# Performance work log

Hardware: AMD Instinct MI355X
Metric: run time of the kernel (lower is better)

The kernel has to match this reference:

```python
import jax, jax.numpy as jnp
import numpy as np

G = 64      # num graphs
N = 1024    # nodes per graph (equal-sized graphs)
D_IN, D_H, D_OUT = 128, 256, 10


def setup_inputs() -> dict:
    key = jax.random.key(0)
    k1, k2, k3, k4, k5 = jax.random.split(key, 5)
    x = jax.random.normal(k1, (G * N, D_IN), dtype=jnp.float32)
    batch = jnp.repeat(jnp.arange(G, dtype=jnp.int64), N)  # sorted graph ids
    lim1 = 1.0 / np.sqrt(D_IN)
    lim2 = 1.0 / np.sqrt(D_H)
    W1 = jax.random.uniform(k2, (D_IN, D_H), minval=-lim1, maxval=lim1, dtype=jnp.float32)
    b1 = jax.random.uniform(k3, (D_H,), minval=-lim1, maxval=lim1, dtype=jnp.float32)
    W2 = jax.random.uniform(k4, (D_H, D_OUT), minval=-lim2, maxval=lim2, dtype=jnp.float32)
    b2 = jax.random.uniform(k5, (D_OUT,), minval=-lim2, maxval=lim2, dtype=jnp.float32)
    return {"x": x, "batch": batch, "W1": W1, "b1": b1, "W2": W2, "b2": b2}


def reference(x, batch, W1, b1, W2, b2):
    # Equal-sized graphs: reshape node dim into [G, N, d] (batch is sorted).
    xg = x.reshape(G, N, D_IN)
    # Cosine-similarity adjacency per graph, zero diagonal (from RAW features).
    xn = xg * jax.lax.rsqrt(jnp.sum(xg * xg, axis=-1, keepdims=True) + 1e-24)
    adj = jnp.einsum('gnd,gmd->gnm', xn, xn)            # [G, N, N]
    adj = adj * (1.0 - jnp.eye(N, dtype=adj.dtype))
    # fc1 + relu on node features, then adjacency propagation.
    h = jax.nn.relu(xg @ W1 + b1)                       # [G, N, D_H]
    h = jnp.einsum('gnm,gmd->gnd', adj, h)              # [G, N, D_H]
    # fc2, global mean pool over nodes, log-softmax over classes.
    out = h @ W2 + b2                                   # [G, N, D_OUT]
    pooled = jnp.mean(out, axis=1)                      # [G, D_OUT]
    return jax.nn.log_softmax(pooled, axis=-1)
```

## Files before the change

### kernel.cpp

```cpp
#include <hip/hip_runtime.h>

#define G_ 64
#define N_ 1024
#define DIN 128
#define DH 256
#define DOUT 10

typedef float floatx4 __attribute__((ext_vector_type(4)));
typedef short shortx8 __attribute__((ext_vector_type(8)));

__device__ __forceinline__ ushort f2bf(float f) {
  unsigned u = __builtin_bit_cast(unsigned, f);
  unsigned r = (u + 0x7FFFu + ((u >> 16) & 1u)) >> 16;
  return (ushort)r;
}
__device__ __forceinline__ float bflo(unsigned q) {
  return __builtin_bit_cast(float, q << 16);
}
__device__ __forceinline__ float bfhi(unsigned q) {
  return __builtin_bit_cast(float, q & 0xFFFF0000u);
}

__global__ __launch_bounds__(256) void k1(
    const float* __restrict__ x, const float* __restrict__ W1,
    ushort* __restrict__ xb, ushort* __restrict__ w1t,
    float* __restrict__ u_part, float* __restrict__ norminv) {
  const int bid = blockIdx.x;
  const int tid = threadIdx.x;
  const int wave = tid >> 6;
  const int lane = tid & 63;
  const int m0 = bid << 7;

  __shared__ float red[4][DIN];

  if (bid < DIN)
    w1t[(size_t)tid * DIN + bid] = f2bf(W1[(size_t)bid * DH + tid]);

  float a0 = 0.f, a1 = 0.f;
  for (int i = 0; i < 32; ++i) {
    const int nb = (wave << 5) + i;
    const int m = m0 + nb;
    const float2 v = ((const float2*)(x + (size_t)m * DIN))[lane];
    float ss = v.x * v.x + v.y * v.y;
    #pragma unroll
    for (int off = 32; off; off >>= 1) ss += __shfl_xor(ss, off, 64);
    const float ninv = rsqrtf(ss + 1e-24f);
    if (lane == 0) norminv[m] = ninv;
    ((unsigned*)xb)[(size_t)m * (DIN / 2) + lane] =
        (unsigned)f2bf(v.x) | ((unsigned)f2bf(v.y) << 16);
    a0 = fmaf(v.x, ninv, a0);
    a1 = fmaf(v.y, ninv, a1);
  }
  red[wave][2 * lane] = a0;
  red[wave][2 * lane + 1] = a1;
  __syncthreads();
  if (tid < DIN)
    u_part[bid * DIN + tid] =
        red[0][tid] + red[1][tid] + red[2][tid] + red[3][tid];
}

__global__ __launch_bounds__(256) void k2(
    const ushort* __restrict__ xb, const ushort* __restrict__ w1t,
    const float* __restrict__ b1, const float* __restrict__ u_part,
    const float* __restrict__ norminv, float* __restrict__ hw_part) {
  const int bid = blockIdx.x;
  const int tid = threadIdx.x;
  const int wave = tid >> 6;
  const int lane = tid & 63;
  const int g = bid >> 3;
  const int m0 = bid << 7;

  __shared__ float u_lds[DIN];
  __shared__ float s_lds[128];

  if (tid < DIN) {
    float s = 0.f;
    #pragma unroll
    for (int i = 0; i < 8; ++i) s += u_part[((g << 3) + i) * DIN + tid];
    u_lds[tid] = s;
  }
  __syncthreads();

  {
    const int nd = tid >> 1;
    const int half = tid & 1;
    const uint4* xr = (const uint4*)(xb + ((size_t)m0 + nd) * DIN + half * 64);
    float p = 0.f;
    #pragma unroll
    for (int j = 0; j < 8; ++j) {
      const uint4 q = xr[j];
      const float* ub = &u_lds[half * 64 + j * 8];
      p = fmaf(bflo(q.x), ub[0], p); p = fmaf(bfhi(q.x), ub[1], p);
      p = fmaf(bflo(q.y), ub[2], p); p = fmaf(bfhi(q.y), ub[3], p);
      p = fmaf(bflo(q.z), ub[4], p); p = fmaf(bfhi(q.z), ub[5], p);
      p = fmaf(bflo(q.w), ub[6], p); p = fmaf(bfhi(q.w), ub[7], p);
    }
    p += __shfl_xor(p, 1, 64);
    if (!half) s_lds[nd] = p * norminv[m0 + nd] - 1.0f;
  }
  __syncthreads();

  const int quad = lane >> 4;
  const int l16 = lane & 15;

  shortx8 bfr[4][4];
  #pragma unroll
  for (int dt = 0; dt < 4; ++dt) {
    const int d = (wave << 6) + (dt << 4) + l16;
    #pragma unroll
    for (int kt = 0; kt < 4; ++kt)
      bfr[dt][kt] =
          *(const shortx8*)(w1t + (size_t)d * DIN + (kt << 5) + (quad << 3));
  }
  float b1v[4];
  #pragma unroll
  for (int dt = 0; dt < 4; ++dt) b1v[dt] = b1[(wave << 6) + (dt << 4) + l16];

  float wsum[4] = {0.f, 0.f, 0.f, 0.f};
  for (int mt = 0; mt < 8; ++mt) {
    const ushort* ar = xb + ((size_t)m0 + (mt << 4) + l16) * DIN;
    shortx8 af[4];
    #pragma unroll
    for (int kt = 0; kt < 4; ++kt)
      af[kt] = *(const shortx8*)(ar + (kt << 5) + (quad << 3));

    floatx4 acc[4] = {{0.f, 0.f, 0.f, 0.f}, {0.f, 0.f, 0.f, 0.f},
                      {0.f, 0.f, 0.f, 0.f}, {0.f, 0.f, 0.f, 0.f}};
    #pragma unroll
    for (int kt = 0; kt < 4; ++kt)
      #pragma unroll
      for (int dt = 0; dt < 4; ++dt)
        acc[dt] = __builtin_amdgcn_mfma_f32_16x16x32_bf16(af[kt], bfr[dt][kt],
                                                          acc[dt], 0, 0, 0);
    #pragma unroll
    for (int dt = 0; dt < 4; ++dt) {
      float bs = 0.f;
      #pragma unroll
      for (int r = 0; r < 4; ++r) {
        const float h = fmaxf(acc[dt][r] + b1v[dt], 0.f);
        bs = fmaf(s_lds[(mt << 4) + (quad << 2) + r], h, bs);
      }
      wsum[dt] += bs;
    }
  }
  #pragma unroll
  for (int dt = 0; dt < 4; ++dt) {
    float w = wsum[dt];
    w += __shfl_xor(w, 16, 64);
    w += __shfl_xor(w, 32, 64);
    if (quad == 0)
      hw_part[bid * DH + (wave << 6) + (dt << 4) + l16] = w;
  }
}

__global__ __launch_bounds__(256) void k3(
    const float* __restrict__ hw_part, const float* __restrict__ W2,
    const float* __restrict__ b2, float* __restrict__ out) {
  const int g = blockIdx.x;
  const int tid = threadIdx.x;
  __shared__ float hv[DH];
  __shared__ float partial[40];
  __shared__ float pv[DOUT];

  float h = 0.f;
  #pragma unroll
  for (int i = 0; i < 8; ++i) h += hw_part[((g << 3) + i) * DH + tid];
  hv[tid] = h;
  __syncthreads();
  if (tid < 40) {
    const int c = tid % 10, q = tid / 10;
    float a = 0.f;
    #pragma unroll
    for (int k = 0; k < 64; ++k)
      a = fmaf(hv[q * 64 + k], W2[(q * 64 + k) * DOUT + c], a);
    partial[tid] = a;
  }
  __syncthreads();
  if (tid < DOUT) {
    pv[tid] = (partial[tid] + partial[tid + 10] + partial[tid + 20] +
               partial[tid + 30]) * (1.0f / N_) + b2[tid];
  }
  __syncthreads();
  if (tid < DOUT) {
    float mx = pv[0];
    #pragma unroll
    for (int c = 1; c < DOUT; ++c) mx = fmaxf(mx, pv[c]);
    float se = 0.f;
    #pragma unroll
    for (int c = 0; c < DOUT; ++c) se += expf(pv[c] - mx);
    out[g * DOUT + tid] = pv[tid] - (mx + logf(se));
  }
}

extern "C" void kernel_launch(void* const* d_in, const int* in_sizes, int n_in,
                              void* d_out, int out_size, void* d_ws, size_t ws_size,
                              hipStream_t stream) {
  const float* x  = (const float*)d_in[0];
  const float* W1 = (const float*)d_in[2];
  const float* b1 = (const float*)d_in[3];
  const float* W2 = (const float*)d_in[4];
  const float* b2 = (const float*)d_in[5];
  float* out = (float*)d_out;

  ushort* xb  = (ushort*)d_ws;
  ushort* w1t = xb + (size_t)G_ * N_ * DIN;
  float* u_part  = (float*)(w1t + (size_t)DH * DIN);
  float* hw_part = u_part + (size_t)512 * DIN;
  float* norminv = hw_part + (size_t)512 * DH;

  k1<<<512, 256, 0, stream>>>(x, W1, xb, w1t, u_part, norminv);
  k2<<<512, 256, 0, stream>>>(xb, w1t, b1, u_part, norminv, hw_part);
  k3<<<G_, 256, 0, stream>>>(hw_part, W2, b2, out);
}
```

Baseline: 117.0 us.

## Widen k1 loads, double its grid, fuse row-dot into k2 MFMA loop

k1 now reads float4 per lane with two rows per wave, runs 1024 blocks of 64 rows each, and writes 8-byte packed bf16 stores, giving it more parallelism and wider memory accesses. In k2 the separate prepass that reread xb to compute the per-node similarity scalar is removed. That dot product is now computed from the MFMA A-fragments already in registers and redistributed with shuffles, which removes one global read pass and a barrier. The cost is extra registers for the u vector and more shuffle work inside the inner loop.

```diff
diff --git a/kernel.cpp b/kernel.cpp
--- a/kernel.cpp
+++ b/kernel.cpp
@@ -29,34 +29,43 @@
   const int tid = threadIdx.x;
   const int wave = tid >> 6;
   const int lane = tid & 63;
-  const int m0 = bid << 7;
-
-  __shared__ float red[4][DIN];
+  const int half = lane >> 5;
+  const int l32 = lane & 31;
+  const int m0 = bid << 6;
+
+  __shared__ float red[8][DIN];
 
   if (bid < DIN)
     w1t[(size_t)tid * DIN + bid] = f2bf(W1[(size_t)bid * DH + tid]);
 
-  float a0 = 0.f, a1 = 0.f;
-  for (int i = 0; i < 32; ++i) {
-    const int nb = (wave << 5) + i;
-    const int m = m0 + nb;
-    const float2 v = ((const float2*)(x + (size_t)m * DIN))[lane];
-    float ss = v.x * v.x + v.y * v.y;
-    #pragma unroll
-    for (int off = 32; off; off >>= 1) ss += __shfl_xor(ss, off, 64);
+  float a0 = 0.f, a1 = 0.f, a2 = 0.f, a3 = 0.f;
+  #pragma unroll
+  for (int it = 0; it < 8; ++it) {
+    const int m = m0 + (wave << 4) + (it << 1) + half;
+    const float4 v = ((const float4*)(x + (size_t)m * DIN))[l32];
+    float ss = v.x * v.x + v.y * v.y + v.z * v.z + v.w * v.w;
+    #pragma unroll
+    for (int off = 16; off; off >>= 1) ss += __shfl_xor(ss, off, 64);
     const float ninv = rsqrtf(ss + 1e-24f);
-    if (lane == 0) norminv[m] = ninv;
-    ((unsigned*)xb)[(size_t)m * (DIN / 2) + lane] =
-        (unsigned)f2bf(v.x) | ((unsigned)f2bf(v.y) << 16);
+    if (l32 == 0) norminv[m] = ninv;
+    const unsigned lo = (unsigned)f2bf(v.x) | ((unsigned)f2bf(v.y) << 16);
+    const unsigned hi = (unsigned)f2bf(v.z) | ((unsigned)f2bf(v.w) << 16);
+    uint2 pk; pk.x = lo; pk.y = hi;
+    ((uint2*)xb)[(size_t)m * 32 + l32] = pk;
     a0 = fmaf(v.x, ninv, a0);
     a1 = fmaf(v.y, ninv, a1);
-  }
-  red[wave][2 * lane] = a0;
-  red[wave][2 * lane + 1] = a1;
-  __syncthreads();
-  if (tid < DIN)
-    u_part[bid * DIN + tid] =
-        red[0][tid] + red[1][tid] + red[2][tid] + red[3][tid];
+    a2 = fmaf(v.z, ninv, a2);
+    a3 = fmaf(v.w, ninv, a3);
+  }
+  float4 av; av.x = a0; av.y = a1; av.z = a2; av.w = a3;
+  ((float4*)red[(wave << 1) + half])[l32] = av;
+  __syncthreads();
+  if (tid < DIN) {
+    float s = 0.f;
+    #pragma unroll
+    for (int i = 0; i < 8; ++i) s += red[i][tid];
+    u_part[bid * DIN + tid] = s;
+  }
 }
 
 __global__ __launch_bounds__(256) void k2(
@@ -69,76 +78,84 @@
   const int lane = tid & 63;
   const int g = bid >> 3;
   const int m0 = bid << 7;
+  const int quad = lane >> 4;
+  const int l16 = lane & 15;
 
   __shared__ float u_lds[DIN];
-  __shared__ float s_lds[128];
+  __shared__ float ninv_lds[128];
 
   if (tid < DIN) {
     float s = 0.f;
     #pragma unroll
-    for (int i = 0; i < 8; ++i) s += u_part[((g << 3) + i) * DIN + tid];
+    for (int i = 0; i < 16; ++i) s += u_part[((g << 4) + i) * DIN + tid];
     u_lds[tid] = s;
-  }
-  __syncthreads();
-
-  {
-    const int nd = tid >> 1;
-    const int half = tid & 1;
-    const uint4* xr = (const uint4*)(xb + ((size_t)m0 + nd) * DIN + half * 64);
+  } else {
+    ninv_lds[tid - 128] = norminv[m0 + tid - 128];
+  }
+  __syncthreads();
+
+  float uu[4][8];
+  #pragma unroll
+  for (int kt = 0; kt < 4; ++kt)
+    #pragma unroll
+    for (int j = 0; j < 8; ++j) uu[kt][j] = u_lds[(kt << 5) + (quad << 3) + j];
+
+  shortx8 bfr[4][4];
+  #pragma unroll
+  for (int dt = 0; dt < 4; ++dt) {
+    const int d = (wave << 6) + (dt << 4) + l16;
+    #pragma unroll
+    for (int kt = 0; kt < 4; ++kt)
+      bfr[dt][kt] =
+          *(const shortx8*)(w1t + (size_t)d * DIN + (kt << 5) + (quad << 3));
+  }
+  float b1v[4];
+  #pragma unroll
+  for (int dt = 0; dt < 4; ++dt) b1v[dt] = b1[(wave << 6) + (dt << 4) + l16];
+
+  float wsum[4] = {0.f, 0.f, 0.f, 0.f};
+  for (int mt = 0; mt < 8; ++mt) {
+    const ushort* ar = xb + ((size_t)m0 + (mt << 4) + l16) * DIN;
+    shortx8 af[4];
+    #pragma unroll
+    for (int kt = 0; kt < 4; ++kt)
+      af[kt] = *(const shortx8*)(ar + (kt << 5) + (quad << 3));
+
+    floatx4 acc[4] = {{0.f, 0.f, 0.f, 0.f}, {0.f, 0.f, 0.f, 0.f},
+                      {0.f, 0.f, 0.f, 0.f}, {0.f, 0.f, 0.f, 0.f}};
+    #pragma unroll
+    for (int kt = 0; kt < 4; ++kt)
+      #pragma unroll
+      for (int dt = 0; dt < 4; ++dt)
+        acc[dt] = __builtin_amdgcn_mfma_f32_16x16x32_bf16(af[kt], bfr[dt][kt],
+                                                          acc[dt], 0, 0, 0);
+
     float p = 0.f;
     #pragma unroll
-    for (int j = 0; j < 8; ++j) {
-      const uint4 q = xr[j];
-      const float* ub = &u_lds[half * 64 + j * 8];
+    for (int kt = 0; kt < 4; ++kt) {
+      const uint4 q = __builtin_bit_cast(uint4, af[kt]);
+      const float* ub = uu[kt];
       p = fmaf(bflo(q.x), ub[0], p); p = fmaf(bfhi(q.x), ub[1], p);
       p = fmaf(bflo(q.y), ub[2], p); p = fmaf(bfhi(q.y), ub[3], p);
       p = fmaf(bflo(q.z), ub[4], p); p = fmaf(bfhi(q.z), ub[5], p);
       p = fmaf(bflo(q.w), ub[6], p); p = fmaf(bfhi(q.w), ub[7], p);
     }
-    p += __shfl_xor(p, 1, 64);
-    if (!half) s_lds[nd] = p * norminv[m0 + nd] - 1.0f;
-  }
-  __syncthreads();
-
-  const int quad = lane >> 4;
-  const int l16 = lane & 15;
-
-  shortx8 bfr[4][4];
-  #pragma unroll
-  for (int dt = 0; dt < 4; ++dt) {
-    const int d = (wave << 6) + (dt << 4) + l16;
-    #pragma unroll
-    for (int kt = 0; kt < 4; ++kt)
-      bfr[dt][kt] =
-          *(const shortx8*)(w1t + (size_t)d * DIN + (kt << 5) + (quad << 3));
-  }
-  float b1v[4];
-  #pragma unroll
-  for (int dt = 0; dt < 4; ++dt) b1v[dt] = b1[(wave << 6) + (dt << 4) + l16];
-
-  float wsum[4] = {0.f, 0.f, 0.f, 0.f};
-  for (int mt = 0; mt < 8; ++mt) {
-    const ushort* ar = xb + ((size_t)m0 + (mt << 4) + l16) * DIN;
-    shortx8 af[4];
-    #pragma unroll
-    for (int kt = 0; kt < 4; ++kt)
-      af[kt] = *(const shortx8*)(ar + (kt << 5) + (quad << 3));
-
-    floatx4 acc[4] = {{0.f, 0.f, 0.f, 0.f}, {0.f, 0.f, 0.f, 0.f},
-                      {0.f, 0.f, 0.f, 0.f}, {0.f, 0.f, 0.f, 0.f}};
-    #pragma unroll
-    for (int kt = 0; kt < 4; ++kt)
-      #pragma unroll
-      for (int dt = 0; dt < 4; ++dt)
-        acc[dt] = __builtin_amdgcn_mfma_f32_16x16x32_bf16(af[kt], bfr[dt][kt],
-                                                          acc[dt], 0, 0, 0);
+    p += __shfl_xor(p, 16, 64);
+    p += __shfl_xor(p, 32, 64);
+    const float s_l = p * ninv_lds[(mt << 4) + l16] - 1.0f;
+
+    float sv[4];
+    #pragma unroll
+    for (int r = 0; r < 4; ++r)
+      sv[r] = __shfl(s_l, (lane & 48) | ((quad << 2) + r), 64);
+
     #pragma unroll
     for (int dt = 0; dt < 4; ++dt) {
       float bs = 0.f;
       #pragma unroll
       for (int r = 0; r < 4; ++r) {
         const float h = fmaxf(acc[dt][r] + b1v[dt], 0.f);
-        bs = fmaf(s_lds[(mt << 4) + (quad << 2) + r], h, bs);
+        bs = fmaf(sv[r], h, bs);
       }
       wsum[dt] += bs;
     }
@@ -205,10 +222,10 @@
   ushort* xb  = (ushort*)d_ws;
   ushort* w1t = xb + (size_t)G_ * N_ * DIN;
   float* u_part  = (float*)(w1t + (size_t)DH * DIN);
-  float* hw_part = u_part + (size_t)512 * DIN;
+  float* hw_part = u_part + (size_t)1024 * DIN;
   float* norminv = hw_part + (size_t)512 * DH;
 
-  k1<<<512, 256, 0, stream>>>(x, W1, xb, w1t, u_part, norminv);
+  k1<<<1024, 256, 0, stream>>>(x, W1, xb, w1t, u_part, norminv);
   k2<<<512, 256, 0, stream>>>(xb, w1t, b1, u_part, norminv, hw_part);
   k3<<<G_, 256, 0, stream>>>(hw_part, W2, b2, out);
 }
```

Result: faster. 105.9 us (-9.5%).
